# Optimization experiments

Measured on AMD Instinct MI355X. Metric: run time of the kernel, lower is better.

The kernel has to match this reference:

```python
import jax, jax.numpy as jnp
import numpy as np

# init_kwargs
H = 8
DC_STRENGTH = 0.01
DC_BANDWIDTH = 16
STOP_WEIGHT = 8.0

# dims
B, T, S, NMEL, L = 16, 800, 160, 80, 4


def setup_inputs() -> dict:
    key = jax.random.key(0)
    ks = jax.random.split(key, 5)
    # per-sample valid lengths in [T//2, T]; mask = first `length` frames valid
    length = jax.random.randint(ks[0], (B,), T // 2, T + 1, dtype=jnp.int32)
    mask = jnp.arange(T)[None, :] < length[:, None]  # [B, T] bool
    # stop-token probabilities in (0, 1)
    stop_pred = jax.random.uniform(ks[1], (B, T), minval=1e-3, maxval=1.0 - 1e-3)
    mels_pred = jax.random.normal(ks[2], (B, T, NMEL))
    mels_target = jax.random.normal(ks[3], (B, T, NMEL))
    # L decoder layers of attention maps [B*H, S, T], normalized over text axis
    alignments = jax.nn.softmax(jax.random.normal(ks[4], (L, B * H, S, T)), axis=2)
    return {"length": length, "mask": mask, "stop_pred": stop_pred,
            "mels_pred": mels_pred, "mels_target": mels_target,
            "alignments": alignments}


def reference(length, mask, stop_pred, mels_pred, mels_target, alignments):
    maskf = mask.astype(mels_pred.dtype)

    # ---- masked L1 mel loss (mean over all elements, like nn.L1Loss) ----
    mel_loss = jnp.mean(jnp.abs(mels_pred * maskf[..., None] - mels_target))

    # ---- stop BCE loss ----
    # Original: masked_select per sample, target = zeros with last=1,
    # weight = target * stop_weight -> only the LAST masked position
    # contributes stop_weight * (-log p). Torch BCE clamps log at -100.
    Tt = mask.shape[1]
    last_idx = Tt - 1 - jnp.argmax(mask[:, ::-1].astype(jnp.int32), axis=1)  # [B]
    p_last = jnp.take_along_axis(stop_pred, last_idx[:, None], axis=1)[:, 0]
    bce_last = -jnp.maximum(jnp.log(p_last), -100.0)  # target = 1
    stop_loss = STOP_WEIGHT * jnp.sum(bce_last) / jnp.sum(maskf)

    # ---- diagonal constraint ----
    Ll, bh, s, t = alignments.shape
    bsz = bh // H
    al = alignments.reshape(Ll, H, bsz, s, t)  # bh is head-major (view(h, batch, ...))
    k = t // s
    ii = jnp.arange(t)  # decoder time
    jj = jnp.arange(s)  # encoder text position
    # window [max(0, k*i - bw), min(s, k*i + bw)) as a static [S, T] band mask
    band = ((jj[:, None] >= k * ii[None, :] - DC_BANDWIDTH) &
            (jj[:, None] < k * ii[None, :] + DC_BANDWIDTH)).astype(al.dtype)
    smask = (t >= length).astype(al.dtype)  # [B], per-sample mask from original
    dc = jnp.einsum('lhbst,st,b->', al, band, smask)
    dc = dc / (H * jnp.sum(length).astype(al.dtype))

    return mel_loss + stop_loss - DC_STRENGTH * dc
```

## Files before the change

kernel.cpp:

```cpp
#include <hip/hip_runtime.h>
#include <math.h>

constexpr int   Hh    = 8;
constexpr float DC_S  = 0.01f;
constexpr int   DC_BW = 16;
constexpr float STOP_W = 8.0f;
constexpr int Bn = 16, Tn = 800, Sn = 160, NM = 80, Ln = 4;
constexpr int Kk = Tn / Sn;
constexpr int MEL4 = Bn * Tn * NM / 4;
constexpr int DCI  = Ln * Bn * Hh * Sn;
constexpr int NITEMS = MEL4 + DCI;
constexpr int BLK  = 1024;
constexpr int NW   = BLK / 64;
constexpr int PROD = NITEMS / BLK;
constexpr unsigned long long POISON = 0xAAAAAAAAAAAAAAAAULL;

union PU { float2 f2; unsigned long long u; };

__global__ __launch_bounds__(BLK) void loss_one(
    const int*   __restrict__ length,
    const float* __restrict__ stop_pred,
    const float* __restrict__ mels_pred,
    const float* __restrict__ mels_target,
    const float* __restrict__ align,
    unsigned long long* __restrict__ part,
    float*       __restrict__ out)
{
    __shared__ float smel[NW], sdc[NW], sst[NW], sln[NW];

    if (blockIdx.x < (unsigned)PROD) {
        int i = blockIdx.x * BLK + threadIdx.x;
        float mel_acc = 0.f, dc_acc = 0.f;

        if (i < MEL4) {
            int bt = (i * 4) / NM;
            int b  = bt / Tn;
            int t  = bt - b * Tn;
            float4 p = reinterpret_cast<const float4*>(mels_pred)[i];
            float4 g = reinterpret_cast<const float4*>(mels_target)[i];
            float  m = (t < length[b]) ? 1.f : 0.f;
            mel_acc = fabsf(p.x * m - g.x) + fabsf(p.y * m - g.y)
                    + fabsf(p.z * m - g.z) + fabsf(p.w * m - g.w);
        } else {
            int j   = i - MEL4;
            int s   = j % Sn;
            int lbh = j / Sn;
            int bh  = lbh % (Bn * Hh);
            int b   = bh % Bn;
            float sm = (Tn >= length[b]) ? 1.f : 0.f;

            int t_lo = (s < DC_BW) ? 0 : (s - DC_BW) / Kk + 1;
            int t_hi = (s + DC_BW) / Kk + 1;
            int base = t_lo & ~3;
            const float4* r4 = reinterpret_cast<const float4*>(
                align + ((size_t)lbh * Sn + s) * (size_t)Tn + base);
            float4 va = r4[0];
            float4 vb = make_float4(0.f, 0.f, 0.f, 0.f);
            float4 vc = make_float4(0.f, 0.f, 0.f, 0.f);
            if (t_hi > base + 4) vb = r4[1];
            if (t_hi > base + 8) vc = r4[2];
            float v[12] = {va.x, va.y, va.z, va.w,
                           vb.x, vb.y, vb.z, vb.w,
                           vc.x, vc.y, vc.z, vc.w};
            float acc = 0.f;
            #pragma unroll
            for (int q = 0; q < 12; ++q) {
                int t = base + q;
                acc += (t >= t_lo && t < t_hi) ? v[q] : 0.f;
            }
            dc_acc = acc * sm;
        }

        for (int off = 32; off > 0; off >>= 1) {
            mel_acc += __shfl_down(mel_acc, off);
            dc_acc  += __shfl_down(dc_acc,  off);
        }
        int wid = threadIdx.x >> 6;
        if ((threadIdx.x & 63) == 0) { smel[wid] = mel_acc; sdc[wid] = dc_acc; }
        __syncthreads();
        if (threadIdx.x == 0) {
            float ms = 0.f, ds = 0.f;
            #pragma unroll
            for (int w = 0; w < NW; ++w) { ms += smel[w]; ds += sdc[w]; }
            PU pu;
            pu.f2 = make_float2(ms, ds);
            __hip_atomic_store(&part[blockIdx.x], pu.u,
                               __ATOMIC_RELAXED, __HIP_MEMORY_SCOPE_AGENT);
        }
        return;
    }

    float stop_t = 0.f, len_t = 0.f;
    if (threadIdx.x < Bn) {
        int len  = length[threadIdx.x];
        len_t    = (float)len;
        float p  = stop_pred[threadIdx.x * Tn + (len - 1)];
        float lg = logf(p);
        if (lg < -100.f) lg = -100.f;
        stop_t = -lg;
    }

    float m = 0.f, d = 0.f;
    if (threadIdx.x < PROD) {
        PU pu;
        pu.u = __hip_atomic_load(&part[threadIdx.x], __ATOMIC_RELAXED,
                                 __HIP_MEMORY_SCOPE_AGENT);
        while (pu.u == POISON) {
            __builtin_amdgcn_s_sleep(2);
            pu.u = __hip_atomic_load(&part[threadIdx.x], __ATOMIC_RELAXED,
                                     __HIP_MEMORY_SCOPE_AGENT);
        }
        m = pu.f2.x;
        d = pu.f2.y;
    }

    for (int off = 32; off > 0; off >>= 1) {
        m      += __shfl_down(m, off);
        d      += __shfl_down(d, off);
        stop_t += __shfl_down(stop_t, off);
        len_t  += __shfl_down(len_t, off);
    }
    int wid = threadIdx.x >> 6;
    if ((threadIdx.x & 63) == 0) {
        smel[wid] = m; sdc[wid] = d; sst[wid] = stop_t; sln[wid] = len_t;
    }
    __syncthreads();
    if (threadIdx.x == 0) {
        float mel_sum = 0.f, dc_sum = 0.f, stop_s = 0.f, sum_len = 0.f;
        #pragma unroll
        for (int w = 0; w < NW; ++w) {
            mel_sum += smel[w]; dc_sum += sdc[w];
            stop_s  += sst[w];  sum_len += sln[w];
        }
        float mel  = mel_sum / (float)(Bn * Tn * NM);
        float stop = STOP_W * stop_s / sum_len;
        float dc   = dc_sum / ((float)Hh * sum_len);
        out[0] = mel + stop - DC_S * dc;
    }
}

extern "C" void kernel_launch(void* const* d_in, const int* in_sizes, int n_in,
                              void* d_out, int out_size, void* d_ws, size_t ws_size,
                              hipStream_t stream)
{
    const int*   length      = (const int*)  d_in[0];
    const float* stop_pred   = (const float*)d_in[2];
    const float* mels_pred   = (const float*)d_in[3];
    const float* mels_target = (const float*)d_in[4];
    const float* align       = (const float*)d_in[5];
    float* out = (float*)d_out;
    unsigned long long* part = (unsigned long long*)d_ws;

    loss_one<<<PROD + 1, BLK, 0, stream>>>(length, stop_pred, mels_pred,
                                           mels_target, align, part, out);
}
```

Baseline: 10.90 us.

## Process two items per thread, skip masked mel_pred loads, make block 0 the reducer

Each producer block now handles two items per thread, which halves the producer block count. Mel and DC work are split into separate blocks so warps no longer diverge between the two. For masked-out frames the mels_pred load is skipped and |target| is used directly, which cuts read traffic. The consumer is moved to block 0, so it is likely scheduled first and spins while the producers run; this relies on all blocks being co-resident or scheduled in order.

Result: slower. 12.32 us (+13.0%).

```diff
diff --git a/kernel.cpp b/kernel.cpp
--- a/kernel.cpp
+++ b/kernel.cpp
@@ -9,13 +9,62 @@
 constexpr int Kk = Tn / Sn;
 constexpr int MEL4 = Bn * Tn * NM / 4;
 constexpr int DCI  = Ln * Bn * Hh * Sn;
-constexpr int NITEMS = MEL4 + DCI;
 constexpr int BLK  = 1024;
 constexpr int NW   = BLK / 64;
-constexpr int PROD = NITEMS / BLK;
+constexpr int IPB  = 2 * BLK;
+constexpr int MELB = MEL4 / IPB;
+constexpr int DCB  = DCI  / IPB;
+constexpr int PROD = MELB + DCB;
 constexpr unsigned long long POISON = 0xAAAAAAAAAAAAAAAAULL;
 
 union PU { float2 f2; unsigned long long u; };
+
+__device__ inline float mel_item(const int* __restrict__ length,
+                                 const float* __restrict__ mp,
+                                 const float* __restrict__ mt, int i)
+{
+    int bt = (i * 4) / NM;
+    int b  = bt / Tn;
+    int t  = bt - b * Tn;
+    float4 g = reinterpret_cast<const float4*>(mt)[i];
+    if (t < length[b]) {
+        float4 p = reinterpret_cast<const float4*>(mp)[i];
+        return fabsf(p.x - g.x) + fabsf(p.y - g.y)
+             + fabsf(p.z - g.z) + fabsf(p.w - g.w);
+    }
+    return fabsf(g.x) + fabsf(g.y) + fabsf(g.z) + fabsf(g.w);
+}
+
+__device__ inline float dc_item(const int* __restrict__ length,
+                                const float* __restrict__ align, int j)
+{
+    int s   = j % Sn;
+    int lbh = j / Sn;
+    int bh  = lbh % (Bn * Hh);
+    int b   = bh % Bn;
+    float sm = (Tn >= length[b]) ? 1.f : 0.f;
+
+    int t_lo = (s < DC_BW) ? 0 : (s - DC_BW) / Kk + 1;
+    int t_hi = (s + DC_BW) / Kk + 1;
+    int base = t_lo & ~3;
+    const float4* r4 = reinterpret_cast<const float4*>(
+        align + ((size_t)lbh * Sn + s) * (size_t)Tn + base);
+    float4 va = r4[0];
+    float4 vb = make_float4(0.f, 0.f, 0.f, 0.f);
+    float4 vc = make_float4(0.f, 0.f, 0.f, 0.f);
+    if (t_hi > base + 4) vb = r4[1];
+    if (t_hi > base + 8) vc = r4[2];
+    float v[12] = {va.x, va.y, va.z, va.w,
+                   vb.x, vb.y, vb.z, vb.w,
+                   vc.x, vc.y, vc.z, vc.w};
+    float acc = 0.f;
+    #pragma unroll
+    for (int q = 0; q < 12; ++q) {
+        int t = base + q;
+        acc += (t >= t_lo && t < t_hi) ? v[q] : 0.f;
+    }
+    return acc * sm;
+}
 
 __global__ __launch_bounds__(BLK) void loss_one(
     const int*   __restrict__ length,
@@ -28,47 +77,18 @@
 {
     __shared__ float smel[NW], sdc[NW], sst[NW], sln[NW];
 
-    if (blockIdx.x < (unsigned)PROD) {
-        int i = blockIdx.x * BLK + threadIdx.x;
+    if (blockIdx.x > 0) {
+        int pb = blockIdx.x - 1;
         float mel_acc = 0.f, dc_acc = 0.f;
 
-        if (i < MEL4) {
-            int bt = (i * 4) / NM;
-            int b  = bt / Tn;
-            int t  = bt - b * Tn;
-            float4 p = reinterpret_cast<const float4*>(mels_pred)[i];
-            float4 g = reinterpret_cast<const float4*>(mels_target)[i];
-            float  m = (t < length[b]) ? 1.f : 0.f;
-            mel_acc = fabsf(p.x * m - g.x) + fabsf(p.y * m - g.y)
-                    + fabsf(p.z * m - g.z) + fabsf(p.w * m - g.w);
+        if (pb < MELB) {
+            int base = pb * IPB + threadIdx.x;
+            mel_acc = mel_item(length, mels_pred, mels_target, base)
+                    + mel_item(length, mels_pred, mels_target, base + BLK);
         } else {
-            int j   = i - MEL4;
-            int s   = j % Sn;
-            int lbh = j / Sn;
-            int bh  = lbh % (Bn * Hh);
-            int b   = bh % Bn;
-            float sm = (Tn >= length[b]) ? 1.f : 0.f;
-
-            int t_lo = (s < DC_BW) ? 0 : (s - DC_BW) / Kk + 1;
-            int t_hi = (s + DC_BW) / Kk + 1;
-            int base = t_lo & ~3;
-            const float4* r4 = reinterpret_cast<const float4*>(
-                align + ((size_t)lbh * Sn + s) * (size_t)Tn + base);
-            float4 va = r4[0];
-            float4 vb = make_float4(0.f, 0.f, 0.f, 0.f);
-            float4 vc = make_float4(0.f, 0.f, 0.f, 0.f);
-            if (t_hi > base + 4) vb = r4[1];
-            if (t_hi > base + 8) vc = r4[2];
-            float v[12] = {va.x, va.y, va.z, va.w,
-                           vb.x, vb.y, vb.z, vb.w,
-                           vc.x, vc.y, vc.z, vc.w};
-            float acc = 0.f;
-            #pragma unroll
-            for (int q = 0; q < 12; ++q) {
-                int t = base + q;
-                acc += (t >= t_lo && t < t_hi) ? v[q] : 0.f;
-            }
-            dc_acc = acc * sm;
+            int base = (pb - MELB) * IPB + threadIdx.x;
+            dc_acc = dc_item(length, align, base)
+                   + dc_item(length, align, base + BLK);
         }
 
         for (int off = 32; off > 0; off >>= 1) {
@@ -84,7 +104,7 @@
             for (int w = 0; w < NW; ++w) { ms += smel[w]; ds += sdc[w]; }
             PU pu;
             pu.f2 = make_float2(ms, ds);
-            __hip_atomic_store(&part[blockIdx.x], pu.u,
+            __hip_atomic_store(&part[pb], pu.u,
                                __ATOMIC_RELAXED, __HIP_MEMORY_SCOPE_AGENT);
         }
         return;
```
